# Kernel tuning notes

Hardware: AMD Instinct MI355X
Metric: run time of the kernel (lower is better)

Reference implementation:

```python
import jax, jax.numpy as jnp
import numpy as np

L = 2
K = 9                      # (L+1)^2 spherical coefficients
N_NODES = 10000
N_EDGES = 80000
C_SPH = 64
C_HID = 64
NHEAD = 8
A_ALPHA = 32
A_VAL = 16
C_OUT = 64
S_GATE = 1 + 2 * L         # gate chunks o_s, o_d^l, o_t^l
EXTRA = NHEAD * A_ALPHA + S_GATE * C_HID   # 256 + 320 = 576

# l-primary -> m-primary permutation for L=2 (m=0 block, then per m: +m coeffs, -m coeffs)
PERM = np.array([0, 2, 6, 3, 7, 1, 5, 8, 4])
INV_PERM = np.argsort(PERM)
L_IDX = np.array([0, 1, 1, 1, 2, 2, 2, 2, 2])  # l of each l-primary coefficient


def scaled_silu(x):
    return jax.nn.silu(x) * (1.0 / 0.6)


def layer_norm(x, w, b, eps=1e-5):
    mu = jnp.mean(x, axis=-1, keepdims=True)
    var = jnp.var(x, axis=-1, keepdims=True)
    return (x - mu) * jax.lax.rsqrt(var + eps) * w + b


def smooth_leaky_relu(x, alpha=0.2):
    return 0.5 * (1 + alpha) * x + 0.5 * (1 - alpha) * x * (2.0 * jax.nn.sigmoid(x) - 1.0)


def _so2_m(x, W):
    # x: [E,2,nin] (row0=+m coeffs, row1=-m coeffs), W: [nin, 2*ncoef*cout]
    y = jnp.einsum('eri,io->ero', x, W)
    half = W.shape[1] // 2
    yr, yi = y[..., :half], y[..., half:]
    out_r = yr[:, 0] - yi[:, 1]
    out_i = yr[:, 1] + yi[:, 0]
    return jnp.stack([out_r, out_i], axis=1)  # [E,2,ncoef*cout]


def so2_conv(emb, cin, cout, wm0, bm0, wm1, wm2, rad=None, extra=0):
    # emb: [E,K,cin] l-primary; block-diagonal per-m SO(2) convolution
    E = emb.shape[0]
    e = emb[:, PERM, :]
    x0 = e[:, 0:3, :].reshape(E, 3 * cin)
    if rad is not None:
        x0 = x0 * rad[:, :3 * cin]
    x0 = x0 @ wm0 + bm0
    x0_extra = None
    if extra:
        x0_extra = x0[:, :extra]
        x0 = x0[:, extra:]
    out0 = x0.reshape(E, 3, cout)
    x1 = e[:, 3:7, :].reshape(E, 2, 2 * cin)
    if rad is not None:
        x1 = x1 * rad[:, 3 * cin:5 * cin][:, None, :]
    out1 = _so2_m(x1, wm1).reshape(E, 4, cout)
    x2 = e[:, 7:9, :].reshape(E, 2, cin)
    if rad is not None:
        x2 = x2 * rad[:, 5 * cin:6 * cin][:, None, :]
    out2 = _so2_m(x2, wm2).reshape(E, 2, cout)
    out = jnp.concatenate([out0, out1, out2], axis=1)[:, INV_PERM, :]
    return out, x0_extra


def _forward(x, atomic_numbers, edge_distance, edge_index, t_ij, rl_ij, wigner, wigner_inv,
             src_emb, tgt_emb, rad_w1, rad_b1, rad_ln_w, rad_ln_b, rad_w2, rad_b2,
             c1_wm0, c1_bm0, c1_wm1, c1_wm2, ln_a_w, ln_a_b, alpha_dot,
             gata_wh, gata_wx, gata_wt, c2_wm0, c2_bm0, c2_wm1, c2_wm2, proj_w, proj_b):
    src, tgt = edge_index[0], edge_index[1]
    x_edge = jnp.concatenate([edge_distance, src_emb[atomic_numbers[src]], tgt_emb[atomic_numbers[tgt]]], axis=1)
    x_src = x[src]                                   # [E,K,C_SPH] gather
    x_tgt = x[tgt]
    h_j = x_tgt[:, 0, :]                              # neighbour scalar part
    X_j = x_tgt[:, 1:, :]                             # neighbour steerable part
    msg = jnp.concatenate([x_src, x_tgt], axis=2)     # [E,K,2*C_SPH]
    msg = jnp.einsum('eij,ejc->eic', wigner, msg)     # per-edge SO(3) rotation
    # radial function: Linear + LayerNorm + ScaledSiLU + Linear
    r = scaled_silu(layer_norm(x_edge @ rad_w1 + rad_b1, rad_ln_w, rad_ln_b)) @ rad_w2 + rad_b2  # [E,768]
    msg, x0_extra = so2_conv(msg, 2 * C_SPH, C_HID, c1_wm0, c1_bm0, c1_wm1, c1_wm2, rad=r, extra=EXTRA)
    a_size = NHEAD * A_ALPHA
    a = x0_extra[:, :a_size].reshape(-1, NHEAD, A_ALPHA)
    attn_out = x0_extra[:, a_size:]                   # [E, S_GATE*C_HID]
    a = smooth_leaky_relu(layer_norm(a, ln_a_w, ln_a_b))
    alpha = jnp.einsum('ehk,hk->eh', a, alpha_dot)    # [E,H]
    # segment softmax over target nodes (torch_geometric.utils.softmax)
    seg_max = jax.ops.segment_max(alpha, tgt, num_segments=N_NODES)
    ex = jnp.exp(alpha - seg_max[tgt])
    denom = jax.ops.segment_sum(ex, tgt, num_segments=N_NODES)
    alpha = ex / (denom[tgt] + 1e-16)
    attn_out = jnp.mean(alpha, axis=1, keepdims=True) * attn_out
    # GATA value activation: gates o_s, o_d^l, o_t^l applied to h_j, X_j, t_ij*rl_ij
    o_s = attn_out[:, :C_HID]
    o_d = attn_out[:, C_HID:(1 + L) * C_HID].reshape(-1, L, C_HID)
    o_t = attn_out[:, (1 + L) * C_HID:].reshape(-1, L, C_HID)
    h = jax.nn.silu(h_j @ gata_wh)                    # [E,C_HID]
    Xp = jnp.einsum('ekc,cd->ekd', X_j, gata_wx)      # [E,K-1,C_HID]
    tp = jax.nn.silu(t_ij @ gata_wt)                  # [E,C_HID]
    parts = [(o_s * h)[:, None, :]]
    for l in range(1, L + 1):
        lo, hi = l * l - 1, (l + 1) * (l + 1) - 1     # rows of this l within X_j / rl_ij
        parts.append(o_d[:, l - 1, None, :] * Xp[:, lo:hi, :]
                     + o_t[:, l - 1, None, :] * (tp[:, None, :] * rl_ij[:, lo:hi, None]))
    msg = jnp.concatenate(parts, axis=1)              # [E,K,C_HID]
    msg, _ = so2_conv(msg, C_HID, NHEAD * A_VAL, c2_wm0, c2_bm0, c2_wm1, c2_wm2)
    E = msg.shape[0]
    msg = (msg.reshape(E, K, NHEAD, A_VAL) * alpha[:, None, :, None]).reshape(E, K, NHEAD * A_VAL)
    msg = jnp.einsum('eij,ejc->eic', wigner_inv, msg)  # rotate back
    node = jax.ops.segment_sum(msg, tgt, num_segments=N_NODES)  # scatter-add to nodes
    out = jnp.einsum('nki,koi->nko', node, proj_w[L_IDX])        # SO3_LinearV2 (per-l weights)
    return out.at[:, 0, :].add(proj_b)


def setup_inputs() -> dict:
    key = jax.random.key(0)
    ks = iter(jax.random.split(key, 48))
    def nrm(shape, scale=1.0):
        return jax.random.normal(next(ks), shape, dtype=jnp.float32) * scale
    inp = {}
    inp['x'] = nrm([N_NODES, K, C_SPH])
    inp['atomic_numbers'] = jax.random.randint(next(ks), (N_NODES,), 0, 100)
    inp['edge_distance'] = nrm([N_EDGES, 64])
    inp['edge_index'] = jax.random.randint(next(ks), (2, N_EDGES), 0, N_NODES)
    inp['t_ij'] = nrm([N_EDGES, 128])
    inp['rl_ij'] = nrm([N_EDGES, K - 1])
    inp['wigner'] = nrm([N_EDGES, K, K], 1.0 / 3.0)
    inp['wigner_inv'] = nrm([N_EDGES, K, K], 1.0 / 3.0)
    inp['src_emb'] = nrm([100, 128], 0.001)
    inp['tgt_emb'] = nrm([100, 128], 0.001)
    inp['rad_w1'] = nrm([320, 128], 320 ** -0.5)
    inp['rad_b1'] = jnp.zeros([128], jnp.float32)
    inp['rad_ln_w'] = jnp.ones([128], jnp.float32)
    inp['rad_ln_b'] = jnp.zeros([128], jnp.float32)
    inp['rad_w2'] = nrm([128, 768], 128 ** -0.5)
    inp['rad_b2'] = jnp.zeros([768], jnp.float32)
    inp['c1_wm0'] = nrm([384, EXTRA + 3 * C_HID], 384 ** -0.5)
    inp['c1_bm0'] = jnp.zeros([EXTRA + 3 * C_HID], jnp.float32)
    inp['c1_wm1'] = nrm([256, 256], 256 ** -0.5)
    inp['c1_wm2'] = nrm([128, 128], 128 ** -0.5)
    inp['ln_a_w'] = jnp.ones([A_ALPHA], jnp.float32)
    inp['ln_a_b'] = jnp.zeros([A_ALPHA], jnp.float32)
    inp['alpha_dot'] = nrm([NHEAD, A_ALPHA], A_ALPHA ** -0.5)
    inp['gata_wh'] = nrm([C_SPH, C_HID], C_SPH ** -0.5)
    inp['gata_wx'] = nrm([C_SPH, C_HID], C_SPH ** -0.5)
    inp['gata_wt'] = nrm([128, C_HID], 128 ** -0.5)
    inp['c2_wm0'] = nrm([3 * C_HID, 3 * NHEAD * A_VAL], (3 * C_HID) ** -0.5)
    inp['c2_bm0'] = jnp.zeros([3 * NHEAD * A_VAL], jnp.float32)
    inp['c2_wm1'] = nrm([2 * C_HID, 2 * NHEAD * A_VAL * 2], (2 * C_HID) ** -0.5)
    inp['c2_wm2'] = nrm([C_HID, 2 * NHEAD * A_VAL], C_HID ** -0.5)
    inp['proj_w'] = nrm([L + 1, C_OUT, NHEAD * A_VAL], (NHEAD * A_VAL) ** -0.5)
    inp['proj_b'] = jnp.zeros([C_OUT], jnp.float32)
    return inp


def reference(x, atomic_numbers, edge_distance, edge_index, t_ij, rl_ij, wigner, wigner_inv,
              src_emb, tgt_emb, rad_w1, rad_b1, rad_ln_w, rad_ln_b, rad_w2, rad_b2,
              c1_wm0, c1_bm0, c1_wm1, c1_wm2, ln_a_w, ln_a_b, alpha_dot,
              gata_wh, gata_wx, gata_wt, c2_wm0, c2_bm0, c2_wm1, c2_wm2, proj_w, proj_b):
    return _forward(x, atomic_numbers, edge_distance, edge_index, t_ij, rl_ij, wigner, wigner_inv,
                    src_emb, tgt_emb, rad_w1, rad_b1, rad_ln_w, rad_ln_b, rad_w2, rad_b2,
                    c1_wm0, c1_bm0, c1_wm1, c1_wm2, ln_a_w, ln_a_b, alpha_dot,
                    gata_wh, gata_wx, gata_wt, c2_wm0, c2_bm0, c2_wm1, c2_wm2, proj_w, proj_b)
```

## Files before the change

### kernel.cpp

```cpp
#include <hip/hip_runtime.h>

#define E_CNT 80000
#define N_NODES 10000

typedef __attribute__((ext_vector_type(8))) __bf16 bf16x8;
typedef __attribute__((ext_vector_type(4))) float f32x4;

__device__ __forceinline__ float sigmoidf_(float x) { return 1.f / (1.f + __expf(-x)); }

__device__ __forceinline__ unsigned fkey(float f) {
  unsigned u = __float_as_uint(f);
  return (u & 0x80000000u) ? ~u : (u | 0x80000000u);
}
__device__ __forceinline__ float unfkey(unsigned k) {
  unsigned u = (k & 0x80000000u) ? (k & 0x7FFFFFFFu) : ~k;
  return __uint_as_float(u);
}

__global__ __launch_bounds__(256) void k_cvt(const float* __restrict__ src,
                                             __bf16* __restrict__ dst,
                                             int K8, int N, int ld) {
  int idx = blockIdx.x * 256 + threadIdx.x;
  if (idx >= K8 * N) return;
  int ksg = idx / N, col = idx % N;
#pragma unroll
  for (int j = 0; j < 8; ++j)
    dst[(size_t)idx * 8 + j] = (__bf16)src[(size_t)(ksg * 8 + j) * ld + col];
}

__global__ __launch_bounds__(256) void k_cvt1(const float* __restrict__ w1,
                                              __bf16* __restrict__ dst) {
  int idx = blockIdx.x * 256 + threadIdx.x;
  if (idx >= 32 * 512) return;
  int ksg = idx >> 9, col = idx & 511;
  int o = col >> 7, c = col & 127;
  const int tc[4] = {0, 128, 256, 384};
  const int bc[4] = {256, 384, 0, 128};
  const float sg[4] = {-1.f, -1.f, 1.f, 1.f};
#pragma unroll
  for (int j = 0; j < 8; ++j) {
    int kk = ksg * 8 + j;
    float v = (kk < 128) ? w1[(size_t)kk * 512 + tc[o] + c]
                         : sg[o] * w1[(size_t)(kk - 128) * 512 + bc[o] + c];
    dst[(size_t)idx * 8 + j] = (__bf16)v;
  }
}

__global__ __launch_bounds__(256) void k_cvt2(const float* __restrict__ w2,
                                              __bf16* __restrict__ dst) {
  int idx = blockIdx.x * 256 + threadIdx.x;
  if (idx >= 16 * 256) return;
  int ksg = idx >> 8, col = idx & 255;
  int o = col >> 7, c = col & 127;
#pragma unroll
  for (int j = 0; j < 8; ++j) {
    int kk = ksg * 8 + j;
    float v;
    if (kk < 64) v = w2[(size_t)kk * 256 + (o == 0 ? c : c + 128)];
    else         v = (o == 0) ? -w2[(size_t)(kk - 64) * 256 + c + 128]
                              :  w2[(size_t)(kk - 64) * 256 + c];
    dst[(size_t)idx * 8 + j] = (__bf16)v;
  }
}

__global__ __launch_bounds__(256, 4) void k_phase1(
    const float* __restrict__ x, const int* __restrict__ an,
    const float* __restrict__ edist, const int* __restrict__ eidx,
    const float* __restrict__ wigner,
    const float* __restrict__ semb, const float* __restrict__ temb,
    const __bf16* __restrict__ rw1f, const float* __restrict__ rb1,
    const float* __restrict__ rlnw, const float* __restrict__ rlnb,
    const __bf16* __restrict__ rw2f, const float* __restrict__ rb2,
    const __bf16* __restrict__ w0r, const float* __restrict__ b0,
    const float* __restrict__ lnaw, const float* __restrict__ lnab,
    const float* __restrict__ adot,
    float* __restrict__ ws_attn, float* __restrict__ ws_apre)
{
  __shared__ __align__(16) float pool[6160];
  __shared__ __align__(16) float bufB[3136];
  __shared__ float wgs[432];
  __shared__ int sidx[16], tidx[16], ansh[16], anth[16];

  const int tid = threadIdx.x;
  const int e0 = blockIdx.x * 16;
  const int lane = tid & 63, wv4 = tid >> 6;
  const int erow = lane & 15, g = lane >> 4;

  __bf16* xe_bf = (__bf16*)pool;
  float* sb = bufB;
  __bf16* sb_bf = (__bf16*)(bufB + 2112);
  __bf16* a_lds2 = (__bf16*)bufB;

  if (tid < 16) {
    int s = eidx[e0 + tid], t = eidx[E_CNT + e0 + tid];
    sidx[tid] = s; tidx[tid] = t; ansh[tid] = an[s]; anth[tid] = an[t];
  }
  for (int i = tid; i < 432; i += 256) {
    int e = i / 27, r = i % 27, kk = r / 9, j = r % 9;
    int row = (kk == 0) ? 0 : (kk == 1 ? 2 : 6);
    wgs[i] = wigner[(size_t)(e0 + e) * 81 + row * 9 + j];
  }
  __syncthreads();

  for (int i = tid; i < 16 * 320; i += 256) {
    int e = i / 320, c = i % 320;
    float v;
    if (c < 64)       v = edist[(size_t)(e0 + e) * 64 + c];
    else if (c < 192) v = semb[ansh[e] * 128 + (c - 64)];
    else              v = temb[anth[e] * 128 + (c - 192)];
    xe_bf[(((c >> 3) * 16 + e) << 3) + (c & 7)] = (__bf16)v;
  }
  __syncthreads();

  {
    bf16x8 af2[10];
#pragma unroll
    for (int ks = 0; ks < 10; ++ks)
      af2[ks] = *(const bf16x8*)(xe_bf + ((ks * 4 + g) * 16 + erow) * 8);
#pragma unroll 1
    for (int tt = 0; tt < 2; ++tt) {
      int col = (wv4 * 2 + tt) * 16 + erow;
      f32x4 acc = {0.f, 0.f, 0.f, 0.f};
#pragma unroll
      for (int ks = 0; ks < 10; ++ks)
        acc = __builtin_amdgcn_mfma_f32_16x16x32_bf16(
            af2[ks], *(const bf16x8*)(rw1f + ((size_t)((ks * 4 + g) * 128) + col) * 8), acc, 0, 0, 0);
      float bb = rb1[col];
#pragma unroll
      for (int r = 0; r < 4; ++r) sb[(g * 4 + r) * 132 + col] = acc[r] + bb;
    }
  }
  __syncthreads();

  {
    int wid = tid >> 6, ln = tid & 63;
    for (int e = wid; e < 16; e += 4) {
      float v0 = sb[e * 132 + ln], v1 = sb[e * 132 + ln + 64];
      float s1 = v0 + v1, s2 = v0 * v0 + v1 * v1;
#pragma unroll
      for (int m = 32; m >= 1; m >>= 1) {
        s1 += __shfl_xor(s1, m);
        s2 += __shfl_xor(s2, m);
      }
      float mu = s1 * (1.f / 128.f);
      float var = s2 * (1.f / 128.f) - mu * mu;
      float rstd = rsqrtf(var + 1e-5f);
      float y0 = (v0 - mu) * rstd * rlnw[ln] + rlnb[ln];
      float y1 = (v1 - mu) * rstd * rlnw[ln + 64] + rlnb[ln + 64];
      sb[e * 132 + ln]      = y0 * sigmoidf_(y0) * (1.f / 0.6f);
      sb[e * 132 + ln + 64] = y1 * sigmoidf_(y1) * (1.f / 0.6f);
    }
  }
  __syncthreads();

  {
    int ksg = tid >> 4, e = tid & 15;
    const float* sp = sb + e * 132 + ksg * 8;
    float4 u0 = *(const float4*)sp;
    float4 u1 = *(const float4*)(sp + 4);
    bf16x8 v;
    v[0] = (__bf16)u0.x; v[1] = (__bf16)u0.y; v[2] = (__bf16)u0.z; v[3] = (__bf16)u0.w;
    v[4] = (__bf16)u1.x; v[5] = (__bf16)u1.y; v[6] = (__bf16)u1.z; v[7] = (__bf16)u1.w;
    *(bf16x8*)(sb_bf + (ksg * 16 + e) * 8) = v;
  }
  __syncthreads();

  float* rbuf = pool;
  {
    bf16x8 af3[4];
#pragma unroll
    for (int ks = 0; ks < 4; ++ks)
      af3[ks] = *(const bf16x8*)(sb_bf + ((ks * 4 + g) * 16 + erow) * 8);
#pragma unroll 1
    for (int tt = 0; tt < 6; ++tt) {
      int col = (wv4 * 6 + tt) * 16 + erow;
      f32x4 acc = {0.f, 0.f, 0.f, 0.f};
#pragma unroll
      for (int ks = 0; ks < 4; ++ks)
        acc = __builtin_amdgcn_mfma_f32_16x16x32_bf16(
            af3[ks], *(const bf16x8*)(rw2f + ((size_t)((ks * 4 + g) * 384) + col) * 8), acc, 0, 0, 0);
      float bb = rb2[col];
#pragma unroll
      for (int r = 0; r < 4; ++r) rbuf[(g * 4 + r) * 385 + col] = acc[r] + bb;
    }
  }
  __syncthreads();

  {
    int e = tid & 15, cg = tid >> 4;
    int c0 = cg * 8;
    const float* xb = (c0 < 64) ? (x + (size_t)sidx[e] * 576 + c0)
                                : (x + (size_t)tidx[e] * 576 + (c0 - 64));
    float xc[9][8];
#pragma unroll
    for (int j = 0; j < 9; ++j) {
      float4 u0 = *(const float4*)(xb + j * 64);
      float4 u1 = *(const float4*)(xb + j * 64 + 4);
      xc[j][0] = u0.x; xc[j][1] = u0.y; xc[j][2] = u0.z; xc[j][3] = u0.w;
      xc[j][4] = u1.x; xc[j][5] = u1.y; xc[j][6] = u1.z; xc[j][7] = u1.w;
    }
#pragma unroll
    for (int kk = 0; kk < 3; ++kk) {
      float wv[9];
#pragma unroll
      for (int j = 0; j < 9; ++j) wv[j] = wgs[e * 27 + kk * 9 + j];
      __bf16* ap = a_lds2 + ((kk * 16 + cg) * 16 + e) * 8;
#pragma unroll
      for (int cu = 0; cu < 8; ++cu) {
        float m = 0.f;
#pragma unroll
        for (int j = 0; j < 9; ++j) m += wv[j] * xc[j][cu];
        int colc = kk * 128 + c0 + cu;
        ap[cu] = (__bf16)(m * rbuf[e * 385 + colc]);
      }
    }
  }
  __syncthreads();

  float* sb5 = pool;
  {
    bf16x8 af[12];
#pragma unroll
    for (int ks = 0; ks < 12; ++ks)
      af[ks] = *(const bf16x8*)(a_lds2 + ((ks * 4 + g) * 16 + erow) * 8);
#pragma unroll 1
    for (int tt = 0; tt < 9; ++tt) {
      int tile = wv4 * 9 + tt;
      int col = tile * 16 + erow;
      f32x4 acc = {0.f, 0.f, 0.f, 0.f};
#pragma unroll
      for (int ks = 0; ks < 12; ++ks) {
        bf16x8 bf = *(const bf16x8*)(w0r + ((size_t)((ks * 4 + g) * 576) + col) * 8);
        acc = __builtin_amdgcn_mfma_f32_16x16x32_bf16(af[ks], bf, acc, 0, 0, 0);
      }
      if (tile < 16) {
#pragma unroll
        for (int r = 0; r < 4; ++r) sb5[(g * 4 + r) * 260 + col] = acc[r];
      } else {
        float bb = b0[col];
#pragma unroll
        for (int r = 0; r < 4; ++r)
          ws_attn[(size_t)(e0 + g * 4 + r) * 320 + (col - 256)] = acc[r] + bb;
      }
    }
  }
  __syncthreads();

  {
    float bb = b0[tid];
    int h = tid >> 5, kk = tid & 31;
    float lw = lnaw[kk], lb = lnab[kk], ad = adot[h * 32 + kk];
#pragma unroll
    for (int e = 0; e < 16; ++e) {
      float v = sb5[e * 260 + tid] + bb;
      float s1 = v, s2 = v * v;
#pragma unroll
      for (int m = 16; m >= 1; m >>= 1) {
        s1 += __shfl_xor(s1, m);
        s2 += __shfl_xor(s2, m);
      }
      float mu = s1 * (1.f / 32.f);
      float var = s2 * (1.f / 32.f) - mu * mu;
      float rstd = rsqrtf(var + 1e-5f);
      float xn = (v - mu) * rstd * lw + lb;
      float sl = 0.6f * xn + 0.4f * xn * (2.f * sigmoidf_(xn) - 1.f);
      float p = sl * ad;
#pragma unroll
      for (int m = 16; m >= 1; m >>= 1) p += __shfl_xor(p, m);
      if (kk == 0) ws_apre[(size_t)(e0 + e) * 8 + h] = p;
    }
  }
}

__global__ __launch_bounds__(256) void k_segmax(const float* __restrict__ apre,
                                                const int* __restrict__ eidx,
                                                unsigned* __restrict__ segk) {
  int idx = blockIdx.x * 256 + threadIdx.x;
  if (idx >= E_CNT * 8) return;
  int e = idx >> 3, h = idx & 7;
  int t = eidx[E_CNT + e];
  atomicMax(&segk[t * 8 + h], fkey(apre[idx]));
}

__global__ __launch_bounds__(256) void k_expsum(const float* __restrict__ apre,
                                                const int* __restrict__ eidx,
                                                const unsigned* __restrict__ segk,
                                                float* __restrict__ ex_out,
                                                float* __restrict__ denom) {
  int idx = blockIdx.x * 256 + threadIdx.x;
  if (idx >= E_CNT * 8) return;
  int e = idx >> 3, h = idx & 7;
  int t = eidx[E_CNT + e];
  float m = unfkey(segk[t * 8 + h]);
  float ex = __expf(apre[idx] - m);
  ex_out[idx] = ex;
  atomicAdd(&denom[t * 8 + h], ex);
}

__global__ __launch_bounds__(256, 3) void k_phase2(
    const float* __restrict__ x, const int* __restrict__ eidx,
    const float* __restrict__ t_ij, const float* __restrict__ rl_ij,
    const float* __restrict__ winv,
    const __bf16* __restrict__ gwhf, const __bf16* __restrict__ gwxf, const __bf16* __restrict__ gwtf,
    const __bf16* __restrict__ w0b, const float* __restrict__ b0,
    const __bf16* __restrict__ w1n, const __bf16* __restrict__ w2n,
    const float* __restrict__ ws_attn, const float* __restrict__ ws_ex,
    const float* __restrict__ denom,
    float* __restrict__ node)
{
  __shared__ __align__(16) __bf16 mb[9 * 8 * 16 * 8];
  __shared__ __align__(16) __bf16 tbf[16 * 16 * 8];
  __shared__ __align__(16) __bf16 xpl[8 * 16 * 64];
  __shared__ __align__(16) __bf16 hl[16 * 64];
  __shared__ __align__(16) __bf16 tpl[16 * 64];
  __shared__ float wib[16 * 81];
  __shared__ float alp[128];
  __shared__ float rlb[128];
  __shared__ float malp[16];
  __shared__ int tnode[16];

  const int tid = threadIdx.x;
  const int e0 = blockIdx.x * 16;
  const int lane = tid & 63, wv = tid >> 6;
  const int e16 = lane & 15, g = lane >> 4;

  if (tid < 16) tnode[tid] = eidx[E_CNT + e0 + tid];
  __syncthreads();

  if (tid < 128) {
    int e = tid >> 3, h = tid & 7;
    float ex = ws_ex[(size_t)(e0 + e) * 8 + h];
    alp[tid] = ex / (denom[tnode[e] * 8 + h] + 1e-16f);
  } else {
    int i = tid - 128;
    rlb[i] = rl_ij[(size_t)(e0 + (i >> 3)) * 8 + (i & 7)];
  }
  for (int i = tid; i < 16 * 81; i += 256)
    wib[i] = winv[(size_t)(e0 + i / 81) * 81 + i % 81];

  for (int i = tid; i < 1152; i += 256) {
    int e = i / 72, rk = i % 72;
    const float* sp = x + (size_t)tnode[e] * 576 + rk * 8;
    float4 u0 = *(const float4*)sp;
    float4 u1 = *(const float4*)(sp + 4);
    bf16x8 v;
    v[0] = (__bf16)u0.x; v[1] = (__bf16)u0.y; v[2] = (__bf16)u0.z; v[3] = (__bf16)u0.w;
    v[4] = (__bf16)u1.x; v[5] = (__bf16)u1.y; v[6] = (__bf16)u1.z; v[7] = (__bf16)u1.w;
    *(bf16x8*)(mb + ((size_t)rk * 16 + e) * 8) = v;
  }
  {
    int e = tid >> 4, ksg = tid & 15;
    const float* sp = t_ij + (size_t)(e0 + e) * 128 + ksg * 8;
    float4 u0 = *(const float4*)sp;
    float4 u1 = *(const float4*)(sp + 4);
    bf16x8 v;
    v[0] = (__bf16)u0.x; v[1] = (__bf16)u0.y; v[2] = (__bf16)u0.z; v[3] = (__bf16)u0.w;
    v[4] = (__bf16)u1.x; v[5] = (__bf16)u1.y; v[6] = (__bf16)u1.z; v[7] = (__bf16)u1.w;
    *(bf16x8*)(tbf + ((size_t)ksg * 16 + e) * 8) = v;
  }
  __syncthreads();
  if (tid < 16) {
    float s = 0.f;
#pragma unroll
    for (int h = 0; h < 8; ++h) s += alp[tid * 8 + h];
    malp[tid] = s * 0.125f;
  }
  __syncthreads();

  {
#define MF(a, b, acc) acc = __builtin_amdgcn_mfma_f32_16x16x32_bf16(a, b, acc, 0, 0, 0)
#define MBF(row, ksg) (*(const bf16x8*)(mb + (((row) * 8 + (ksg)) * 16 + e16) * 8))
#define TBF(ksg) (*(const bf16x8*)(tbf + ((ksg) * 16 + e16) * 8))
#define XPROW(rr)                                                              \
  {                                                                            \
    _Pragma("unroll 1")                                                        \
    for (int q = 0; q < 4; ++q) {                                              \
      f32x4 acc = {0.f, 0.f, 0.f, 0.f};                                        \
      MF(MBF(rr, g),                                                           \
         *(const bf16x8*)(gwxf + ((size_t)(g * 64) + q * 16 + e16) * 8), acc); \
      MF(MBF(rr, 4 + g),                                                       \
         *(const bf16x8*)(gwxf + ((size_t)((4 + g) * 64) + q * 16 + e16) * 8), acc); \
      _Pragma("unroll")                                                        \
      for (int r = 0; r < 4; ++r)                                              \
        xpl[(((rr) - 1) * 16 + (g * 4 + r)) * 64 + q * 16 + e16] = (__bf16)acc[r]; \
    }                                                                          \
  }
    if (wv == 0) {
#pragma unroll 1
      for (int q = 0; q < 4; ++q) {
        f32x4 acc = {0.f, 0.f, 0.f, 0.f};
#pragma unroll
        for (int ks = 0; ks < 4; ++ks)
          MF(TBF(ks * 4 + g),
             *(const bf16x8*)(gwtf + ((size_t)((ks * 4 + g) * 64) + q * 16 + e16) * 8), acc);
#pragma unroll
        for (int r = 0; r < 4; ++r) {
          float v = acc[r];
          tpl[(g * 4 + r) * 64 + q * 16 + e16] = (__bf16)(v * sigmoidf_(v));
        }
      }
      XPROW(1)
    } else if (wv == 1) {
#pragma unroll 1
      for (int q = 0; q < 4; ++q) {
        f32x4 acc = {0.f, 0.f, 0.f, 0.f};
        MF(MBF(0, g),
           *(const bf16x8*)(gwhf + ((size_t)(g * 64) + q * 16 + e16) * 8), acc);
        MF(MBF(0, 4 + g),
           *(const bf16x8*)(gwhf + ((size_t)((4 + g) * 64) + q * 16 + e16) * 8), acc);
#pragma unroll
        for (int r = 0; r < 4; ++r) {
          float v = acc[r];
          hl[(g * 4 + r) * 64 + q * 16 + e16] = (__bf16)(v * sigmoidf_(v));
        }
      }
      XPROW(2)
      XPROW(3)
    } else if (wv == 2) {
      XPROW(4)
      XPROW(5)
      XPROW(6)
    } else {
      XPROW(7)
      XPROW(8)
    }
#undef XPROW
#undef TBF
  }
  __syncthreads();

  {
    int d = tid & 63, wid = tid >> 6;
    int dk = d >> 3, dj = d & 7;
#pragma unroll
    for (int i = 0; i < 4; ++i) {
      int e = wid * 4 + i;
      float ml = malp[e];
      const float* wsb = ws_attn + (size_t)(e0 + e) * 320;
      float os  = wsb[d] * ml;
      float od0 = wsb[64 + d] * ml,  od1 = wsb[128 + d] * ml;
      float ot0 = wsb[192 + d] * ml, ot1 = wsb[256 + d] * ml;
      float hv = (float)hl[e * 64 + d];
      float tv = (float)tpl[e * 64 + d];
      mb[((0 * 8 + dk) * 16 + e) * 8 + dj] = (__bf16)(os * hv);
#pragma unroll
      for (int j = 0; j < 3; ++j) {
        float xv = (float)xpl[(j * 16 + e) * 64 + d];
        mb[(((1 + j) * 8 + dk) * 16 + e) * 8 + dj] =
            (__bf16)(od0 * xv + ot0 * tv * rlb[e * 8 + j]);
      }
#pragma unroll
      for (int j = 0; j < 5; ++j) {
        float xv = (float)xpl[((3 + j) * 16 + e) * 64 + d];
        mb[(((4 + j) * 8 + dk) * 16 + e) * 8 + dj] =
            (__bf16)(od1 * xv + ot1 * tv * rlb[e * 8 + 3 + j]);
      }
    }
  }
  __syncthreads();

  {
#define AF(row, ks) (*(const bf16x8*)(mb + (((row) * 8 + (ks)) * 16 + e16) * 8))
#define MF2(a, b, acc) acc = __builtin_amdgcn_mfma_f32_16x16x32_bf16(a, b, acc, 0, 0, 0)
#pragma unroll 1
    for (int gi = 0; gi < 2; ++gi) {
      const int c = (wv * 2 + gi) * 16 + e16;
      const int h = c >> 4;
      const float av0 = alp[(g * 4 + 0) * 8 + h];
      const float av1 = alp[(g * 4 + 1) * 8 + h];
      const float av2 = alp[(g * 4 + 2) * 8 + h];
      const float av3 = alp[(g * 4 + 3) * 8 + h];
      const float* wp0 = wib + (g * 4 + 0) * 81;
      const float* wp1 = wib + (g * 4 + 1) * 81;
      const float* wp2 = wib + (g * 4 + 2) * 81;
      const float* wp3 = wib + (g * 4 + 3) * 81;
      f32x4 oa[9];
#pragma unroll
      for (int i = 0; i < 9; ++i) oa[i] = (f32x4){0.f, 0.f, 0.f, 0.f};

      {
        bf16x8 a0 = AF(0, g), a1 = AF(0, 4 + g);
        bf16x8 a2 = AF(2, g), a3 = AF(2, 4 + g);
        bf16x8 a4 = AF(6, g), a5 = AF(6, 4 + g);
#pragma unroll 1
        for (int o = 0; o < 3; ++o) {
          const __bf16* wp = w0b + ((size_t)(g * 384) + o * 128 + c) * 8;
          f32x4 acc = {0.f, 0.f, 0.f, 0.f};
          MF2(a0, *(const bf16x8*)(wp + (size_t)0 * 4 * 384 * 8), acc);
          MF2(a1, *(const bf16x8*)(wp + (size_t)1 * 4 * 384 * 8), acc);
          MF2(a2, *(const bf16x8*)(wp + (size_t)2 * 4 * 384 * 8), acc);
          MF2(a3, *(const bf16x8*)(wp + (size_t)3 * 4 * 384 * 8), acc);
          MF2(a4, *(const bf16x8*)(wp + (size_t)4 * 4 * 384 * 8), acc);
          MF2(a5, *(const bf16x8*)(wp + (size_t)5 * 4 * 384 * 8), acc);
          const int j = (o == 0) ? 0 : (o == 1) ? 2 : 6;
          const float bb = b0[o * 128 + c];
          const float t0 = (acc[0] + bb) * av0;
          const float t1 = (acc[1] + bb) * av1;
          const float t2 = (acc[2] + bb) * av2;
          const float t3 = (acc[3] + bb) * av3;
#pragma unroll
          for (int i = 0; i < 9; ++i) {
            oa[i][0] += wp0[i * 9 + j] * t0;
            oa[i][1] += wp1[i * 9 + j] * t1;
            oa[i][2] += wp2[i * 9 + j] * t2;
            oa[i][3] += wp3[i * 9 + j] * t3;
          }
        }
      }
      {
        bf16x8 a0 = AF(3, g), a1 = AF(3, 4 + g);
        bf16x8 a2 = AF(7, g), a3 = AF(7, 4 + g);
        bf16x8 a4 = AF(1, g), a5 = AF(1, 4 + g);
        bf16x8 a6 = AF(5, g), a7 = AF(5, 4 + g);
#pragma unroll 1
        for (int o = 0; o < 4; ++o) {
          const __bf16* wp = w1n + ((size_t)(g * 512) + o * 128 + c) * 8;
          f32x4 acc = {0.f, 0.f, 0.f, 0.f};
          MF2(a0, *(const bf16x8*)(wp + (size_t)0 * 4 * 512 * 8), acc);
          MF2(a1, *(const bf16x8*)(wp + (size_t)1 * 4 * 512 * 8), acc);
          MF2(a2, *(const bf16x8*)(wp + (size_t)2 * 4 * 512 * 8), acc);
          MF2(a3, *(const bf16x8*)(wp + (size_t)3 * 4 * 512 * 8), acc);
          MF2(a4, *(const bf16x8*)(wp + (size_t)4 * 4 * 512 * 8), acc);
          MF2(a5, *(const bf16x8*)(wp + (size_t)5 * 4 * 512 * 8), acc);
          MF2(a6, *(const bf16x8*)(wp + (size_t)6 * 4 * 512 * 8), acc);
          MF2(a7, *(const bf16x8*)(wp + (size_t)7 * 4 * 512 * 8), acc);
          const int j = (o == 0) ? 3 : (o == 1) ? 7 : (o == 2) ? 1 : 5;
          const float t0 = acc[0] * av0;
          const float t1 = acc[1] * av1;
          const float t2 = acc[2] * av2;
          const float t3 = acc[3] * av3;
#pragma unroll
          for (int i = 0; i < 9; ++i) {
            oa[i][0] += wp0[i * 9 + j] * t0;
            oa[i][1] += wp1[i * 9 + j] * t1;
            oa[i][2] += wp2[i * 9 + j] * t2;
            oa[i][3] += wp3[i * 9 + j] * t3;
          }
        }
      }
      {
        bf16x8 a0 = AF(8, g), a1 = AF(8, 4 + g);
        bf16x8 a2 = AF(4, g), a3 = AF(4, 4 + g);
#pragma unroll 1
        for (int o = 0; o < 2; ++o) {
          const __bf16* wp = w2n + ((size_t)(g * 256) + o * 128 + c) * 8;
          f32x4 acc = {0.f, 0.f, 0.f, 0.f};
          MF2(a0, *(const bf16x8*)(wp + (size_t)0 * 4 * 256 * 8), acc);
          MF2(a1, *(const bf16x8*)(wp + (size_t)1 * 4 * 256 * 8), acc);
          MF2(a2, *(const bf16x8*)(wp + (size_t)2 * 4 * 256 * 8), acc);
          MF2(a3, *(const bf16x8*)(wp + (size_t)3 * 4 * 256 * 8), acc);
          const int j = (o == 0) ? 8 : 4;
          const float t0 = acc[0] * av0;
          const float t1 = acc[1] * av1;
          const float t2 = acc[2] * av2;
          const float t3 = acc[3] * av3;
#pragma unroll
          for (int i = 0; i < 9; ++i) {
            oa[i][0] += wp0[i * 9 + j] * t0;
            oa[i][1] += wp1[i * 9 + j] * t1;
            oa[i][2] += wp2[i * 9 + j] * t2;
            oa[i][3] += wp3[i * 9 + j] * t3;
          }
        }
      }
#pragma unroll
      for (int r = 0; r < 4; ++r) {
        float* np = node + (size_t)tnode[g * 4 + r] * 1152 + c;
#pragma unroll
        for (int i = 0; i < 9; ++i) atomicAdd(np + i * 128, oa[i][r]);
      }
    }
#undef MF2
#undef AF
#undef MBF
#undef MF
  }
}

__global__ __launch_bounds__(256) void k_wt(const float* __restrict__ pw, float* __restrict__ wT) {
  int idx = blockIdx.x * 256 + threadIdx.x;
  if (idx >= 3 * 128 * 64) return;
  int l = idx / 8192, r = idx % 8192, i = r / 64, o = r % 64;
  wT[idx] = pw[(l * 64 + o) * 128 + i];
}

__global__ __launch_bounds__(256) void k_proj(const float* __restrict__ node,
                                              const float* __restrict__ wT,
                                              const float* __restrict__ pb,
                                              float* __restrict__ out) {
  __shared__ __align__(16) float A[32 * 132];
  int k = blockIdx.y;
  int n0 = blockIdx.x * 32;
  const int lidx = (k == 0) ? 0 : (k <= 3 ? 1 : 2);
  int tid = threadIdx.x;
  for (int i = tid; i < 32 * 128; i += 256) {
    int nn = i >> 7, ii = i & 127;
    int n = n0 + nn;
    A[nn * 132 + ii] = (n < N_NODES) ? node[((size_t)n * 9 + k) * 128 + ii] : 0.f;
  }
  __syncthreads();
  int o = tid & 63, wid = tid >> 6;
  float acc[8] = {0.f, 0.f, 0.f, 0.f, 0.f, 0.f, 0.f, 0.f};
#pragma unroll 4
  for (int i = 0; i < 128; ++i) {
    float w = wT[lidx * 8192 + i * 64 + o];
#pragma unroll
    for (int r = 0; r < 8; ++r) acc[r] += A[(wid * 8 + r) * 132 + i] * w;
  }
  float bias = (k == 0) ? pb[o] : 0.f;
#pragma unroll
  for (int r = 0; r < 8; ++r) {
    int n = n0 + wid * 8 + r;
    if (n < N_NODES) out[((size_t)n * 9 + k) * 64 + o] = acc[r] + bias;
  }
}

extern "C" void kernel_launch(void* const* d_in, const int* in_sizes, int n_in,
                              void* d_out, int out_size, void* d_ws, size_t ws_size,
                              hipStream_t stream) {
  const float* x      = (const float*)d_in[0];
  const int*   an     = (const int*)d_in[1];
  const float* edist  = (const float*)d_in[2];
  const int*   eidx   = (const int*)d_in[3];
  const float* t_ij   = (const float*)d_in[4];
  const float* rl_ij  = (const float*)d_in[5];
  const float* wig    = (const float*)d_in[6];
  const float* winv   = (const float*)d_in[7];
  const float* semb   = (const float*)d_in[8];
  const float* temb   = (const float*)d_in[9];
  const float* rw1    = (const float*)d_in[10];
  const float* rb1    = (const float*)d_in[11];
  const float* rlnw   = (const float*)d_in[12];
  const float* rlnb   = (const float*)d_in[13];
  const float* rw2    = (const float*)d_in[14];
  const float* rb2    = (const float*)d_in[15];
  const float* c1w0   = (const float*)d_in[16];
  const float* c1b0   = (const float*)d_in[17];
  const float* lnaw   = (const float*)d_in[20];
  const float* lnab   = (const float*)d_in[21];
  const float* adot   = (const float*)d_in[22];
  const float* gwh    = (const float*)d_in[23];
  const float* gwx    = (const float*)d_in[24];
  const float* gwt    = (const float*)d_in[25];
  const float* c2w0   = (const float*)d_in[26];
  const float* c2b0   = (const float*)d_in[27];
  const float* c2w1   = (const float*)d_in[28];
  const float* c2w2   = (const float*)d_in[29];
  const float* pw     = (const float*)d_in[30];
  const float* pb     = (const float*)d_in[31];
  float* out = (float*)d_out;

  char* p = (char*)d_ws;
  float* ws_attn  = (float*)p; p += (size_t)E_CNT * 320 * 4;
  float* ws_apre  = (float*)p; p += (size_t)E_CNT * 8 * 4;
  float* ws_ex    = (float*)p; p += (size_t)E_CNT * 8 * 4;
  unsigned* segk  = (unsigned*)p; p += (size_t)N_NODES * 8 * 4;
  float* denom    = (float*)p; p += (size_t)N_NODES * 8 * 4;
  float* node     = (float*)p; p += (size_t)N_NODES * 1152 * 4;
  float* wT       = (float*)p; p += (size_t)3 * 128 * 64 * 4;
  __bf16* w0r     = (__bf16*)p; p += (size_t)48 * 576 * 8 * 2;
  __bf16* w0b     = (__bf16*)p; p += (size_t)24 * 384 * 8 * 2;
  __bf16* w1n     = (__bf16*)p; p += (size_t)32 * 512 * 8 * 2;
  __bf16* w2n     = (__bf16*)p; p += (size_t)16 * 256 * 8 * 2;
  __bf16* rw1f    = (__bf16*)p; p += (size_t)40 * 128 * 8 * 2;
  __bf16* rw2f    = (__bf16*)p; p += (size_t)16 * 384 * 8 * 2;
  __bf16* gwhf    = (__bf16*)p; p += (size_t)8 * 64 * 8 * 2;
  __bf16* gwxf    = (__bf16*)p; p += (size_t)8 * 64 * 8 * 2;
  __bf16* gwtf    = (__bf16*)p; p += (size_t)16 * 64 * 8 * 2;

  hipMemsetAsync(segk, 0, N_NODES * 8 * 4, stream);
  hipMemsetAsync(denom, 0, N_NODES * 8 * 4, stream);
  hipMemsetAsync(node, 0, (size_t)N_NODES * 1152 * 4, stream);

  k_cvt<<<108, 256, 0, stream>>>(c1w0, w0r, 48, 576, 768);
  k_cvt<<<36, 256, 0, stream>>>(c2w0, w0b, 24, 384, 384);
  k_cvt1<<<64, 256, 0, stream>>>(c2w1, w1n);
  k_cvt2<<<16, 256, 0, stream>>>(c2w2, w2n);
  k_cvt<<<20, 256, 0, stream>>>(rw1, rw1f, 40, 128, 128);
  k_cvt<<<24, 256, 0, stream>>>(rw2, rw2f, 16, 384, 768);
  k_cvt<<<2, 256, 0, stream>>>(gwh, gwhf, 8, 64, 64);
  k_cvt<<<2, 256, 0, stream>>>(gwx, gwxf, 8, 64, 64);
  k_cvt<<<4, 256, 0, stream>>>(gwt, gwtf, 16, 64, 64);
  k_wt<<<96, 256, 0, stream>>>(pw, wT);
  k_phase1<<<E_CNT / 16, 256, 0, stream>>>(x, an, edist, eidx, wig, semb, temb,
                                           rw1f, rb1, rlnw, rlnb, rw2f, rb2,
                                           w0r, c1b0, lnaw, lnab, adot,
                                           ws_attn, ws_apre);
  k_segmax<<<(E_CNT * 8) / 256, 256, 0, stream>>>(ws_apre, eidx, segk);
  k_expsum<<<(E_CNT * 8) / 256, 256, 0, stream>>>(ws_apre, eidx, segk, ws_ex, denom);
  k_phase2<<<E_CNT / 16, 256, 0, stream>>>(x, eidx, t_ij, rl_ij, winv,
                                           gwhf, gwxf, gwtf, w0b, c2b0, w1n, w2n,
                                           ws_attn, ws_ex, denom, node);
  k_proj<<<dim3((N_NODES + 31) / 32, 9), 256, 0, stream>>>(node, wT, pb, out);
}
```

Baseline: 816.7 us.

## Keep gate projections in registers and fuse gating into MFMA epilogue

The gate projections (h, t, and the x rows) are now computed per wave over a 16-channel slice, so each wave owns the full set of 9 rows for its channels and keeps the results in registers. The separate shared-memory staging buffers (xpl, hl, tpl) and the pass that recombined them are removed; gating is applied directly in the MFMA epilogue and the results are written back into mb after a barrier. This cuts LDS traffic and shared-memory footprint, which lets the occupancy hint rise from 3 to 4 blocks per CU. The cost is higher register pressure from the nine held accumulators, which the tighter launch bound could turn into spills.

```diff
diff --git a/kernel.cpp b/kernel.cpp
--- a/kernel.cpp
+++ b/kernel.cpp
@@ -297,7 +297,7 @@
   atomicAdd(&denom[t * 8 + h], ex);
 }
 
-__global__ __launch_bounds__(256, 3) void k_phase2(
+__global__ __launch_bounds__(256, 4) void k_phase2(
     const float* __restrict__ x, const int* __restrict__ eidx,
     const float* __restrict__ t_ij, const float* __restrict__ rl_ij,
     const float* __restrict__ winv,
@@ -310,9 +310,6 @@
 {
   __shared__ __align__(16) __bf16 mb[9 * 8 * 16 * 8];
   __shared__ __align__(16) __bf16 tbf[16 * 16 * 8];
-  __shared__ __align__(16) __bf16 xpl[8 * 16 * 64];
-  __shared__ __align__(16) __bf16 hl[16 * 64];
-  __shared__ __align__(16) __bf16 tpl[16 * 64];
   __shared__ float wib[16 * 81];
   __shared__ float alp[128];
   __shared__ float rlb[128];
@@ -367,95 +364,83 @@
   }
   __syncthreads();
 
-  {
+  f32x4 M0, M1, M2, M3, M4, M5, M6, M7, M8;
+  {
+    const int c = wv * 16 + e16;
 #define MF(a, b, acc) acc = __builtin_amdgcn_mfma_f32_16x16x32_bf16(a, b, acc, 0, 0, 0)
 #define MBF(row, ksg) (*(const bf16x8*)(mb + (((row) * 8 + (ksg)) * 16 + e16) * 8))
-#define TBF(ksg) (*(const bf16x8*)(tbf + ((ksg) * 16 + e16) * 8))
-#define XPROW(rr)                                                              \
-  {                                                                            \
-    _Pragma("unroll 1")                                                        \
-    for (int q = 0; q < 4; ++q) {                                              \
-      f32x4 acc = {0.f, 0.f, 0.f, 0.f};                                        \
-      MF(MBF(rr, g),                                                           \
-         *(const bf16x8*)(gwxf + ((size_t)(g * 64) + q * 16 + e16) * 8), acc); \
-      MF(MBF(rr, 4 + g),                                                       \
-         *(const bf16x8*)(gwxf + ((size_t)((4 + g) * 64) + q * 16 + e16) * 8), acc); \
-      _Pragma("unroll")                                                        \
-      for (int r = 0; r < 4; ++r)                                              \
-        xpl[(((rr) - 1) * 16 + (g * 4 + r)) * 64 + q * 16 + e16] = (__bf16)acc[r]; \
-    }                                                                          \
-  }
-    if (wv == 0) {
-#pragma unroll 1
-      for (int q = 0; q < 4; ++q) {
-        f32x4 acc = {0.f, 0.f, 0.f, 0.f};
-#pragma unroll
-        for (int ks = 0; ks < 4; ++ks)
-          MF(TBF(ks * 4 + g),
-             *(const bf16x8*)(gwtf + ((size_t)((ks * 4 + g) * 64) + q * 16 + e16) * 8), acc);
-#pragma unroll
-        for (int r = 0; r < 4; ++r) {
-          float v = acc[r];
-          tpl[(g * 4 + r) * 64 + q * 16 + e16] = (__bf16)(v * sigmoidf_(v));
-        }
-      }
-      XPROW(1)
-    } else if (wv == 1) {
-#pragma unroll 1
-      for (int q = 0; q < 4; ++q) {
-        f32x4 acc = {0.f, 0.f, 0.f, 0.f};
-        MF(MBF(0, g),
-           *(const bf16x8*)(gwhf + ((size_t)(g * 64) + q * 16 + e16) * 8), acc);
-        MF(MBF(0, 4 + g),
-           *(const bf16x8*)(gwhf + ((size_t)((4 + g) * 64) + q * 16 + e16) * 8), acc);
-#pragma unroll
-        for (int r = 0; r < 4; ++r) {
-          float v = acc[r];
-          hl[(g * 4 + r) * 64 + q * 16 + e16] = (__bf16)(v * sigmoidf_(v));
-        }
-      }
-      XPROW(2)
-      XPROW(3)
-    } else if (wv == 2) {
-      XPROW(4)
-      XPROW(5)
-      XPROW(6)
-    } else {
-      XPROW(7)
-      XPROW(8)
-    }
-#undef XPROW
-#undef TBF
-  }
-  __syncthreads();
-
-  {
-    int d = tid & 63, wid = tid >> 6;
-    int dk = d >> 3, dj = d & 7;
-#pragma unroll
-    for (int i = 0; i < 4; ++i) {
-      int e = wid * 4 + i;
+    f32x4 tv4;
+    {
+      f32x4 acc = {0.f, 0.f, 0.f, 0.f};
+#pragma unroll
+      for (int ks = 0; ks < 4; ++ks)
+        MF(*(const bf16x8*)(tbf + ((ks * 4 + g) * 16 + e16) * 8),
+           *(const bf16x8*)(gwtf + ((size_t)((ks * 4 + g) * 64) + c) * 8), acc);
+#pragma unroll
+      for (int r = 0; r < 4; ++r) { float v = acc[r]; tv4[r] = v * sigmoidf_(v); }
+    }
+    f32x4 hv4;
+    {
+      f32x4 acc = {0.f, 0.f, 0.f, 0.f};
+      MF(MBF(0, g), *(const bf16x8*)(gwhf + ((size_t)(g * 64) + c) * 8), acc);
+      MF(MBF(0, 4 + g), *(const bf16x8*)(gwhf + ((size_t)((4 + g) * 64) + c) * 8), acc);
+#pragma unroll
+      for (int r = 0; r < 4; ++r) { float v = acc[r]; hv4[r] = v * sigmoidf_(v); }
+    }
+    f32x4 osv, od0v, od1v, ot0v, ot1v;
+#pragma unroll
+    for (int r = 0; r < 4; ++r) {
+      int e = g * 4 + r;
       float ml = malp[e];
       const float* wsb = ws_attn + (size_t)(e0 + e) * 320;
-      float os  = wsb[d] * ml;
-      float od0 = wsb[64 + d] * ml,  od1 = wsb[128 + d] * ml;
-      float ot0 = wsb[192 + d] * ml, ot1 = wsb[256 + d] * ml;
-      float hv = (float)hl[e * 64 + d];
-      float tv = (float)tpl[e * 64 + d];
-      mb[((0 * 8 + dk) * 16 + e) * 8 + dj] = (__bf16)(os * hv);
-#pragma unroll
-      for (int j = 0; j < 3; ++j) {
-        float xv = (float)xpl[(j * 16 + e) * 64 + d];
-        mb[(((1 + j) * 8 + dk) * 16 + e) * 8 + dj] =
-            (__bf16)(od0 * xv + ot0 * tv * rlb[e * 8 + j]);
-      }
-#pragma unroll
-      for (int j = 0; j < 5; ++j) {
-        float xv = (float)xpl[((3 + j) * 16 + e) * 64 + d];
-        mb[(((4 + j) * 8 + dk) * 16 + e) * 8 + dj] =
-            (__bf16)(od1 * xv + ot1 * tv * rlb[e * 8 + 3 + j]);
-      }
-    }
+      osv[r]  = wsb[c] * ml;
+      od0v[r] = wsb[64 + c] * ml;
+      od1v[r] = wsb[128 + c] * ml;
+      ot0v[r] = wsb[192 + c] * ml;
+      ot1v[r] = wsb[256 + c] * ml;
+    }
+#pragma unroll
+    for (int r = 0; r < 4; ++r) M0[r] = osv[r] * hv4[r];
+    bf16x8 bx0 = *(const bf16x8*)(gwxf + ((size_t)(g * 64) + c) * 8);
+    bf16x8 bx1 = *(const bf16x8*)(gwxf + ((size_t)((4 + g) * 64) + c) * 8);
+#define XROW(rr, MV, odv, otv, jj)                                        \
+    {                                                                     \
+      f32x4 acc = {0.f, 0.f, 0.f, 0.f};                                   \
+      MF(MBF(rr, g), bx0, acc);                                           \
+      MF(MBF(rr, 4 + g), bx1, acc);                                       \
+      _Pragma("unroll")                                                   \
+      for (int r = 0; r < 4; ++r) {                                       \
+        int e = g * 4 + r;                                                \
+        MV[r] = odv[r] * acc[r] + otv[r] * tv4[r] * rlb[e * 8 + (jj)];    \
+      }                                                                   \
+    }
+    XROW(1, M1, od0v, ot0v, 0)
+    XROW(2, M2, od0v, ot0v, 1)
+    XROW(3, M3, od0v, ot0v, 2)
+    XROW(4, M4, od1v, ot1v, 3)
+    XROW(5, M5, od1v, ot1v, 4)
+    XROW(6, M6, od1v, ot1v, 5)
+    XROW(7, M7, od1v, ot1v, 6)
+    XROW(8, M8, od1v, ot1v, 7)
+#undef XROW
+#undef MBF
+  }
+  __syncthreads();
+
+  {
+    const int c = wv * 16 + e16;
+    const int cksg = c >> 3, cj = c & 7;
+#define WOUT(rr, MV)                                                       \
+    {                                                                      \
+      _Pragma("unroll")                                                    \
+      for (int r = 0; r < 4; ++r) {                                        \
+        int e = g * 4 + r;                                                 \
+        mb[(((rr) * 8 + cksg) * 16 + e) * 8 + cj] = (__bf16)MV[r];         \
+      }                                                                    \
+    }
+    WOUT(0, M0) WOUT(1, M1) WOUT(2, M2) WOUT(3, M3) WOUT(4, M4)
+    WOUT(5, M5) WOUT(6, M6) WOUT(7, M7) WOUT(8, M8)
+#undef WOUT
   }
   __syncthreads();
 
@@ -572,7 +557,6 @@
     }
 #undef MF2
 #undef AF
-#undef MBF
 #undef MF
   }
 }
```

Result: slower. 908.9 us (+11.3%).
